# Kernel optimization log

Measured on AMD Instinct MI355X. Metric: run time of the kernel, lower is better.

Reference implementation:

```python
import jax, jax.numpy as jnp
import numpy as np

VOCAB, D = 500000, 128
B, K = 16384, 10          # word-level pairs, negatives per pair
B2, L, W = 8192, 5, 10    # mwe batch, max entity len, 2*window context


def setup_inputs() -> dict:
    key = jax.random.key(0)
    ks = jax.random.split(key, 9)
    scale = 1.0 / np.sqrt(D)
    return {
        "center_table": jax.random.normal(ks[0], (VOCAB, D), jnp.float32) * scale,
        "context_table": jax.random.normal(ks[1], (VOCAB, D), jnp.float32) * scale,
        "w_center": jax.random.randint(ks[2], (B,), 0, VOCAB),
        "w_outside": jax.random.randint(ks[3], (B,), 0, VOCAB),
        "w_neg": jax.random.randint(ks[4], (B, K), 0, VOCAB),
        "m_center": jax.random.randint(ks[5], (B2, L), 0, VOCAB),
        "m_len": jax.random.randint(ks[6], (B2,), 1, L + 1),
        "m_outside": jax.random.randint(ks[7], (B2, W), 0, VOCAB),
        "m_neg": jax.random.randint(ks[8], (B2 * W, K), 0, VOCAB),
    }


def _masked_mean_mwe(emb, lengths):
    # emb: (B2, L, D); masked mean over first `lengths` tokens (mwe_f)
    mask = (jnp.arange(emb.shape[1])[None, :] < lengths[:, None]).astype(emb.dtype)
    return jnp.sum(emb * mask[:, :, None], axis=1) / lengths[:, None].astype(emb.dtype)


def reference(center_table, context_table, w_center, w_outside, w_neg,
              m_center, m_len, m_outside, m_neg):
    ls = jax.nn.log_sigmoid

    # ----- word-level skip-gram negative sampling -----
    ce = center_table[w_center]            # (B, D)
    oe = context_table[w_outside]          # (B, D)
    ne = context_table[w_neg]              # (B, K, D)
    pos = -ls(jnp.sum(oe * ce, axis=-1))                       # (B,)
    neg = jnp.sum(-ls(-jnp.einsum('bkd,bd->bk', ne, ce)), -1)  # (B,)
    loss_words = jnp.mean(pos + neg)

    # ----- MWE skip-gram negative sampling -----
    valid = (m_outside.reshape(-1) != 0)                       # pad token == 0
    mwe = _masked_mean_mwe(center_table[m_center], m_len)      # (B2, D)
    mwe_rep = jnp.broadcast_to(mwe[:, None, :], (B2, W, D)).reshape(-1, D)  # (B2*W, D)
    oe2 = context_table[m_outside.reshape(-1)]                 # (B2*W, D)
    ne2 = context_table[m_neg]                                 # (B2*W, K, D)
    pos2 = -ls(jnp.sum(oe2 * mwe_rep, axis=-1))                           # (B2*W,)
    neg2 = jnp.sum(-ls(-jnp.einsum('nkd,nd->nk', ne2, mwe_rep)), -1)      # (B2*W,)
    vf = valid.astype(pos2.dtype)
    loss_mwes = jnp.sum((pos2 + neg2) * vf) / jnp.maximum(jnp.sum(vf), 1.0)

    return loss_words + 25.0 * loss_mwes
```

## Files before the change

kernel.cpp:

```cpp
#include <hip/hip_runtime.h>
#include <hip/hip_bf16.h>
#include <math.h>

#define DIMD 128
#define NB   16384
#define NK   10
#define NB2  8192
#define NL   5
#define NW   10

__device__ __forceinline__ float softplus_fast(float z) {
  return fmaxf(z, 0.0f) + __logf(1.0f + __expf(-fabsf(z)));
}

__device__ __forceinline__ float rs16(float v[16], int lane) {
  const bool b5 = (lane & 32) != 0, b4 = (lane & 16) != 0;
  const bool b3 = (lane & 8) != 0,  b2 = (lane & 4) != 0;
#pragma unroll
  for (int j = 0; j < 8; ++j) {
    float send = b5 ? v[j] : v[j + 8];
    float recv = __shfl_xor(send, 32);
    v[j] = (b5 ? v[j + 8] : v[j]) + recv;
  }
#pragma unroll
  for (int j = 0; j < 4; ++j) {
    float send = b4 ? v[j] : v[j + 4];
    float recv = __shfl_xor(send, 16);
    v[j] = (b4 ? v[j + 4] : v[j]) + recv;
  }
#pragma unroll
  for (int j = 0; j < 2; ++j) {
    float send = b3 ? v[j] : v[j + 2];
    float recv = __shfl_xor(send, 8);
    v[j] = (b3 ? v[j + 2] : v[j]) + recv;
  }
  {
    float send = b2 ? v[0] : v[1];
    float recv = __shfl_xor(send, 4);
    v[0] = (b2 ? v[1] : v[0]) + recv;
  }
  float s = v[0];
  s += __shfl_xor(s, 2);
  s += __shfl_xor(s, 1);
  return s;
}

__device__ __forceinline__ float wred64(float v) {
  v += __shfl_xor(v, 32);
  v += __shfl_xor(v, 16);
  v += __shfl_xor(v, 8);
  v += __shfl_xor(v, 4);
  v += __shfl_xor(v, 2);
  v += __shfl_xor(v, 1);
  return v;
}

__device__ __forceinline__ float2 row2(const float* __restrict__ tab, int idx, int lane) {
  return *reinterpret_cast<const float2*>(tab + (size_t)idx * DIMD + 2 * lane);
}

__global__ __launch_bounds__(256) void k_words(
    const float* __restrict__ ct, const float* __restrict__ xt,
    const int* __restrict__ wc, const int* __restrict__ wo,
    const int* __restrict__ wn, float* __restrict__ partials) {
  const int tid  = blockIdx.x * 256 + threadIdx.x;
  const int b    = tid >> 6;
  const int lane = threadIdx.x & 63;
  const int   idx   = ((lane >> 5) & 1) * 8 + ((lane >> 4) & 1) * 4 +
                      ((lane >> 3) & 1) * 2 + ((lane >> 2) & 1);
  const float zsgn  = (idx == 0) ? -1.0f : 1.0f;
  const float wmask = (((lane & 3) == 0) && idx <= 10) ? 1.0f : 0.0f;

  const float2 ce = row2(ct, wc[b], lane);
  const float2 oe = row2(xt, wo[b], lane);

  int ni[NK];
#pragma unroll
  for (int k = 0; k < NK; ++k) ni[k] = wn[b * NK + k];
  float2 nv[NK];
#pragma unroll
  for (int k = 0; k < NK; ++k) nv[k] = row2(xt, ni[k], lane);

  float v[16];
  v[0] = ce.x * oe.x + ce.y * oe.y;
#pragma unroll
  for (int k = 0; k < NK; ++k) v[1 + k] = ce.x * nv[k].x + ce.y * nv[k].y;
#pragma unroll
  for (int j = 11; j < 16; ++j) v[j] = 0.0f;

  const float s = rs16(v, lane);
  float wsum = wred64(softplus_fast(s * zsgn) * wmask);

  __shared__ float sm[4];
  if (lane == 0) sm[threadIdx.x >> 6] = wsum;
  __syncthreads();
  if (threadIdx.x == 0)
    partials[blockIdx.x] = (sm[0] + sm[1]) + (sm[2] + sm[3]);
}

__global__ __launch_bounds__(256) void k_mwe(
    const float* __restrict__ ct, const float* __restrict__ xt,
    const int* __restrict__ mc, const int* __restrict__ mlen,
    const int* __restrict__ mo, const int* __restrict__ mn,
    float2* __restrict__ partials) {
  const int tid  = blockIdx.x * 256 + threadIdx.x;
  const int g    = tid >> 6;
  const int lane = threadIdx.x & 63;
  const int   idx   = ((lane >> 5) & 1) * 8 + ((lane >> 4) & 1) * 4 +
                      ((lane >> 3) & 1) * 2 + ((lane >> 2) & 1);
  const float zsgn  = (idx == 0) ? -1.0f : 1.0f;
  const float wmask = (((lane & 3) == 0) && idx <= 10) ? 1.0f : 0.0f;

  const int len = mlen[g];
  float mx = 0.0f, my = 0.0f;
  for (int t = 0; t < len; ++t) {
    const float2 e = row2(ct, mc[g * NL + t], lane);
    mx += e.x; my += e.y;
  }
  const float inv = 1.0f / (float)len;
  mx *= inv; my *= inv;

  float wsum = 0.0f, wcnt = 0.0f;
  for (int w = 0; w < NW; ++w) {
    const int o = mo[g * NW + w];
    if (o == 0) continue;
    const int* __restrict__ nrow = mn + (size_t)(g * NW + w) * NK;
    int ni[NK];
#pragma unroll
    for (int k = 0; k < NK; ++k) ni[k] = nrow[k];
    const float2 oe = row2(xt, o, lane);
    float2 nv[NK];
#pragma unroll
    for (int k = 0; k < NK; ++k) nv[k] = row2(xt, ni[k], lane);

    float v[16];
    v[0] = mx * oe.x + my * oe.y;
#pragma unroll
    for (int k = 0; k < NK; ++k) v[1 + k] = mx * nv[k].x + my * nv[k].y;
#pragma unroll
    for (int j = 11; j < 16; ++j) v[j] = 0.0f;

    const float s = rs16(v, lane);
    wsum += softplus_fast(s * zsgn) * wmask;
    wcnt += 1.0f;
  }

  wsum = wred64(wsum);

  __shared__ float sm[4], sc[4];
  if (lane == 0) { sm[threadIdx.x >> 6] = wsum; sc[threadIdx.x >> 6] = wcnt; }
  __syncthreads();
  if (threadIdx.x == 0)
    partials[blockIdx.x] = make_float2((sm[0] + sm[1]) + (sm[2] + sm[3]),
                                       (sc[0] + sc[1]) + (sc[2] + sc[3]));
}

__global__ __launch_bounds__(256) void k_final(
    const float* __restrict__ wp, const float2* __restrict__ mp,
    float* __restrict__ out) {
  __shared__ float sa[256], sb[256], sc[256];
  float s = 0.0f;
  for (int i = threadIdx.x; i < NB / 4; i += 256) s += wp[i];
  float ms = 0.0f, mcn = 0.0f;
  for (int i = threadIdx.x; i < NB2 / 4; i += 256) {
    const float2 v = mp[i];
    ms += v.x; mcn += v.y;
  }
  sa[threadIdx.x] = s; sb[threadIdx.x] = ms; sc[threadIdx.x] = mcn;
  __syncthreads();
  if (threadIdx.x == 0) {
    float S = 0.0f, MS = 0.0f, MC = 0.0f;
    for (int i = 0; i < 256; ++i) { S += sa[i]; MS += sb[i]; MC += sc[i]; }
    out[0] = S / (float)NB + 25.0f * (MS / fmaxf(MC, 1.0f));
  }
}

extern "C" void kernel_launch(void* const* d_in, const int* in_sizes, int n_in,
                              void* d_out, int out_size, void* d_ws, size_t ws_size,
                              hipStream_t stream) {
  const float* ct   = (const float*)d_in[0];
  const float* xt   = (const float*)d_in[1];
  const int*   wc   = (const int*)d_in[2];
  const int*   wo   = (const int*)d_in[3];
  const int*   wn   = (const int*)d_in[4];
  const int*   mc   = (const int*)d_in[5];
  const int*   mlen = (const int*)d_in[6];
  const int*   mo   = (const int*)d_in[7];
  const int*   mn   = (const int*)d_in[8];

  float*  wp = (float*)d_ws;
  float2* mp = (float2*)(wp + NB / 4);

  k_words<<<NB / 4, 256, 0, stream>>>(ct, xt, wc, wo, wn, wp);
  k_mwe<<<NB2 / 4, 256, 0, stream>>>(ct, xt, mc, mlen, mo, mn, mp);
  k_final<<<1, 256, 0, stream>>>(wp, mp, (float*)d_out);
}
```

Before: 104.8 us.

## Precompute MWE means and fuse word and MWE windows into one flat grid

Adds a separate kernel that computes each entity's masked mean embedding into workspace. A single fused kernel then runs one wavefront per word pair or per MWE window, instead of one wavefront looping serially over all 10 windows. This exposes far more independent gathers in flight and removes the k_words/k_mwe split. In exchange it adds an extra launch plus a write and re-read of the mean buffer, and it launches many more blocks.

```diff
diff --git a/kernel.cpp b/kernel.cpp
--- a/kernel.cpp
+++ b/kernel.cpp
@@ -3,14 +3,22 @@
 #include <math.h>
 
 #define DIMD 128
-#define NB   16384
-#define NK   10
-#define NB2  8192
-#define NL   5
-#define NW   10
+#define NB    16384
+#define NK    10
+#define NB2   8192
+#define NL    5
+#define NW    10
+#define NWIN  (NB2 * NW)
+#define NBLK_W (NB / 4)
+#define NBLK_M (NWIN / 4)
+#define NBLK  (NBLK_W + NBLK_M)
 
 __device__ __forceinline__ float softplus_fast(float z) {
   return fmaxf(z, 0.0f) + __logf(1.0f + __expf(-fabsf(z)));
+}
+
+__device__ __forceinline__ float2 row2(const float* __restrict__ tab, int idx, int lane) {
+  return *reinterpret_cast<const float2*>(tab + (size_t)idx * DIMD + 2 * lane);
 }
 
 __device__ __forceinline__ float rs16(float v[16], int lane) {
@@ -18,25 +26,21 @@
   const bool b3 = (lane & 8) != 0,  b2 = (lane & 4) != 0;
 #pragma unroll
   for (int j = 0; j < 8; ++j) {
-    float send = b5 ? v[j] : v[j + 8];
-    float recv = __shfl_xor(send, 32);
+    float recv = __shfl_xor(b5 ? v[j] : v[j + 8], 32);
     v[j] = (b5 ? v[j + 8] : v[j]) + recv;
   }
 #pragma unroll
   for (int j = 0; j < 4; ++j) {
-    float send = b4 ? v[j] : v[j + 4];
-    float recv = __shfl_xor(send, 16);
+    float recv = __shfl_xor(b4 ? v[j] : v[j + 4], 16);
     v[j] = (b4 ? v[j + 4] : v[j]) + recv;
   }
 #pragma unroll
   for (int j = 0; j < 2; ++j) {
-    float send = b3 ? v[j] : v[j + 2];
-    float recv = __shfl_xor(send, 8);
+    float recv = __shfl_xor(b3 ? v[j] : v[j + 2], 8);
     v[j] = (b3 ? v[j + 2] : v[j]) + recv;
   }
   {
-    float send = b2 ? v[0] : v[1];
-    float recv = __shfl_xor(send, 4);
+    float recv = __shfl_xor(b2 ? v[0] : v[1], 4);
     v[0] = (b2 ? v[1] : v[0]) + recv;
   }
   float s = v[0];
@@ -45,133 +49,110 @@
   return s;
 }
 
-__device__ __forceinline__ float wred64(float v) {
-  v += __shfl_xor(v, 32);
-  v += __shfl_xor(v, 16);
-  v += __shfl_xor(v, 8);
-  v += __shfl_xor(v, 4);
-  v += __shfl_xor(v, 2);
-  v += __shfl_xor(v, 1);
-  return v;
+__device__ __forceinline__ float window_term(
+    const float* __restrict__ xt, float cx, float cy, int pos,
+    const int* __restrict__ nrow, int lane, float zsgn, float wmask) {
+  int ni[NK];
+#pragma unroll
+  for (int k = 0; k < NK; ++k) ni[k] = nrow[k];
+  const float2 oe = row2(xt, pos, lane);
+  float2 nv[NK];
+#pragma unroll
+  for (int k = 0; k < NK; ++k) nv[k] = row2(xt, ni[k], lane);
+
+  float v[16];
+  v[0] = cx * oe.x + cy * oe.y;
+#pragma unroll
+  for (int k = 0; k < NK; ++k) v[1 + k] = cx * nv[k].x + cy * nv[k].y;
+#pragma unroll
+  for (int j = 11; j < 16; ++j) v[j] = 0.0f;
+
+  const float s = rs16(v, lane);
+  return softplus_fast(s * zsgn) * wmask;
 }
 
-__device__ __forceinline__ float2 row2(const float* __restrict__ tab, int idx, int lane) {
-  return *reinterpret_cast<const float2*>(tab + (size_t)idx * DIMD + 2 * lane);
+__global__ __launch_bounds__(256) void k_mean(
+    const float* __restrict__ ct, const int* __restrict__ mc,
+    const int* __restrict__ mlen, float* __restrict__ wsm) {
+  const int tid  = blockIdx.x * 256 + threadIdx.x;
+  const int g    = tid >> 6;
+  const int lane = threadIdx.x & 63;
+  const int len  = mlen[g];
+  int ti[NL];
+#pragma unroll
+  for (int t = 0; t < NL; ++t) ti[t] = mc[g * NL + t];
+  float mx = 0.0f, my = 0.0f;
+#pragma unroll
+  for (int t = 0; t < NL; ++t) {
+    const float2 e = row2(ct, ti[t], lane);
+    if (t < len) { mx += e.x; my += e.y; }
+  }
+  const float inv = 1.0f / (float)len;
+  *reinterpret_cast<float2*>(wsm + (size_t)g * DIMD + 2 * lane) =
+      make_float2(mx * inv, my * inv);
 }
 
-__global__ __launch_bounds__(256) void k_words(
+__global__ __launch_bounds__(256) void k_main(
     const float* __restrict__ ct, const float* __restrict__ xt,
+    const float* __restrict__ wsm,
     const int* __restrict__ wc, const int* __restrict__ wo,
-    const int* __restrict__ wn, float* __restrict__ partials) {
-  const int tid  = blockIdx.x * 256 + threadIdx.x;
-  const int b    = tid >> 6;
+    const int* __restrict__ wn,
+    const int* __restrict__ mo, const int* __restrict__ mn,
+    float2* __restrict__ partials) {
+  const int bid  = blockIdx.x;
+  const int widx = threadIdx.x >> 6;
   const int lane = threadIdx.x & 63;
   const int   idx   = ((lane >> 5) & 1) * 8 + ((lane >> 4) & 1) * 4 +
                       ((lane >> 3) & 1) * 2 + ((lane >> 2) & 1);
   const float zsgn  = (idx == 0) ? -1.0f : 1.0f;
   const float wmask = (((lane & 3) == 0) && idx <= 10) ? 1.0f : 0.0f;
 
-  const float2 ce = row2(ct, wc[b], lane);
-  const float2 oe = row2(xt, wo[b], lane);
+  float term = 0.0f, cnt = 0.0f;
+  if (bid < NBLK_W) {
+    const int b = bid * 4 + widx;
+    const float2 cvec = row2(ct, wc[b], lane);
+    term = window_term(xt, cvec.x, cvec.y, wo[b], wn + (size_t)b * NK,
+                       lane, zsgn, wmask);
+  } else {
+    const int win = (bid - NBLK_W) * 4 + widx;
+    const int o = mo[win];
+    if (o != 0) {
+      const int g = win / NW;
+      const float2 cvec = row2(wsm, g, lane);
+      term = window_term(xt, cvec.x, cvec.y, o, mn + (size_t)win * NK,
+                         lane, zsgn, wmask);
+      cnt = 1.0f;
+    }
+  }
 
-  int ni[NK];
-#pragma unroll
-  for (int k = 0; k < NK; ++k) ni[k] = wn[b * NK + k];
-  float2 nv[NK];
-#pragma unroll
-  for (int k = 0; k < NK; ++k) nv[k] = row2(xt, ni[k], lane);
+  term += __shfl_xor(term, 4);
+  term += __shfl_xor(term, 8);
+  term += __shfl_xor(term, 16);
+  term += __shfl_xor(term, 32);
 
-  float v[16];
-  v[0] = ce.x * oe.x + ce.y * oe.y;
-#pragma unroll
-  for (int k = 0; k < NK; ++k) v[1 + k] = ce.x * nv[k].x + ce.y * nv[k].y;
-#pragma unroll
-  for (int j = 11; j < 16; ++j) v[j] = 0.0f;
-
-  const float s = rs16(v, lane);
-  float wsum = wred64(softplus_fast(s * zsgn) * wmask);
-
-  __shared__ float sm[4];
-  if (lane == 0) sm[threadIdx.x >> 6] = wsum;
+  __shared__ float sm[4], sc[4];
+  if (lane == 0) { sm[widx] = term; sc[widx] = cnt; }
   __syncthreads();
   if (threadIdx.x == 0)
-    partials[blockIdx.x] = (sm[0] + sm[1]) + (sm[2] + sm[3]);
-}
-
-__global__ __launch_bounds__(256) void k_mwe(
-    const float* __restrict__ ct, const float* __restrict__ xt,
-    const int* __restrict__ mc, const int* __restrict__ mlen,
-    const int* __restrict__ mo, const int* __restrict__ mn,
-    float2* __restrict__ partials) {
-  const int tid  = blockIdx.x * 256 + threadIdx.x;
-  const int g    = tid >> 6;
-  const int lane = threadIdx.x & 63;
-  const int   idx   = ((lane >> 5) & 1) * 8 + ((lane >> 4) & 1) * 4 +
-                      ((lane >> 3) & 1) * 2 + ((lane >> 2) & 1);
-  const float zsgn  = (idx == 0) ? -1.0f : 1.0f;
-  const float wmask = (((lane & 3) == 0) && idx <= 10) ? 1.0f : 0.0f;
-
-  const int len = mlen[g];
-  float mx = 0.0f, my = 0.0f;
-  for (int t = 0; t < len; ++t) {
-    const float2 e = row2(ct, mc[g * NL + t], lane);
-    mx += e.x; my += e.y;
-  }
-  const float inv = 1.0f / (float)len;
-  mx *= inv; my *= inv;
-
-  float wsum = 0.0f, wcnt = 0.0f;
-  for (int w = 0; w < NW; ++w) {
-    const int o = mo[g * NW + w];
-    if (o == 0) continue;
-    const int* __restrict__ nrow = mn + (size_t)(g * NW + w) * NK;
-    int ni[NK];
-#pragma unroll
-    for (int k = 0; k < NK; ++k) ni[k] = nrow[k];
-    const float2 oe = row2(xt, o, lane);
-    float2 nv[NK];
-#pragma unroll
-    for (int k = 0; k < NK; ++k) nv[k] = row2(xt, ni[k], lane);
-
-    float v[16];
-    v[0] = mx * oe.x + my * oe.y;
-#pragma unroll
-    for (int k = 0; k < NK; ++k) v[1 + k] = mx * nv[k].x + my * nv[k].y;
-#pragma unroll
-    for (int j = 11; j < 16; ++j) v[j] = 0.0f;
-
-    const float s = rs16(v, lane);
-    wsum += softplus_fast(s * zsgn) * wmask;
-    wcnt += 1.0f;
-  }
-
-  wsum = wred64(wsum);
-
-  __shared__ float sm[4], sc[4];
-  if (lane == 0) { sm[threadIdx.x >> 6] = wsum; sc[threadIdx.x >> 6] = wcnt; }
-  __syncthreads();
-  if (threadIdx.x == 0)
-    partials[blockIdx.x] = make_float2((sm[0] + sm[1]) + (sm[2] + sm[3]),
-                                       (sc[0] + sc[1]) + (sc[2] + sc[3]));
+    partials[bid] = make_float2((sm[0] + sm[1]) + (sm[2] + sm[3]),
+                                (sc[0] + sc[1]) + (sc[2] + sc[3]));
 }
 
 __global__ __launch_bounds__(256) void k_final(
-    const float* __restrict__ wp, const float2* __restrict__ mp,
-    float* __restrict__ out) {
+    const float2* __restrict__ partials, float* __restrict__ out) {
   __shared__ float sa[256], sb[256], sc[256];
-  float s = 0.0f;
-  for (int i = threadIdx.x; i < NB / 4; i += 256) s += wp[i];
-  float ms = 0.0f, mcn = 0.0f;
-  for (int i = threadIdx.x; i < NB2 / 4; i += 256) {
-    const float2 v = mp[i];
-    ms += v.x; mcn += v.y;
+  float S = 0.0f, MS = 0.0f, MC = 0.0f;
+  for (int i = threadIdx.x; i < NBLK_W; i += 256) S += partials[i].x;
+  for (int i = NBLK_W + threadIdx.x; i < NBLK; i += 256) {
+    const float2 v = partials[i];
+    MS += v.x; MC += v.y;
   }
-  sa[threadIdx.x] = s; sb[threadIdx.x] = ms; sc[threadIdx.x] = mcn;
+  sa[threadIdx.x] = S; sb[threadIdx.x] = MS; sc[threadIdx.x] = MC;
   __syncthreads();
   if (threadIdx.x == 0) {
-    float S = 0.0f, MS = 0.0f, MC = 0.0f;
-    for (int i = 0; i < 256; ++i) { S += sa[i]; MS += sb[i]; MC += sc[i]; }
-    out[0] = S / (float)NB + 25.0f * (MS / fmaxf(MC, 1.0f));
+    float s = 0.0f, ms = 0.0f, mc2 = 0.0f;
+    for (int i = 0; i < 256; ++i) { s += sa[i]; ms += sb[i]; mc2 += sc[i]; }
+    out[0] = s / (float)NB + 25.0f * (ms / fmaxf(mc2, 1.0f));
   }
 }
 
@@ -188,10 +169,10 @@
   const int*   mo   = (const int*)d_in[7];
   const int*   mn   = (const int*)d_in[8];
 
-  float*  wp = (float*)d_ws;
-  float2* mp = (float2*)(wp + NB / 4);
+  float*  wsm      = (float*)d_ws;
+  float2* partials = (float2*)(wsm + (size_t)NB2 * DIMD);
 
-  k_words<<<NB / 4, 256, 0, stream>>>(ct, xt, wc, wo, wn, wp);
-  k_mwe<<<NB2 / 4, 256, 0, stream>>>(ct, xt, mc, mlen, mo, mn, mp);
-  k_final<<<1, 256, 0, stream>>>(wp, mp, (float*)d_out);
+  k_mean<<<NB2 / 4, 256, 0, stream>>>(ct, mc, mlen, wsm);
+  k_main<<<NBLK, 256, 0, stream>>>(ct, xt, wsm, wc, wo, wn, mo, mn, partials);
+  k_final<<<1, 256, 0, stream>>>(partials, (float*)d_out);
 }
```

Result: slower. 116.6 us (+11.3%).
